# Kernel tuning notes

Measured on AMD Instinct MI355X. Metric: run time of the kernel, lower is better.

## Reference

```python
import jax, jax.numpy as jnp
import numpy as np

B, N = 2048, 4095  # batch, number of spherical points (cumsum length = N+1)


def setup_inputs() -> dict:
    key = jax.random.key(0)
    k1, k2, k3, k4, k5 = jax.random.split(key, 5)
    return {
        "origin_3D": jax.random.uniform(k1, (B, 3, 1), dtype=jnp.float32),
        "spherical_3D": jax.random.uniform(k2, (B, 3, N), dtype=jnp.float32),
        "origin_2D": jax.random.uniform(k3, (B, 3, 1), dtype=jnp.float32),
        "spherical_2D": jax.random.uniform(k4, (B, 3, N), dtype=jnp.float32),
        "deformation_field": jax.random.uniform(k5, (B, 2, N), dtype=jnp.float32),
    }


def _cart(origin, spherical):
    # spherical: [B, 3, N] with rows (r, theta, phi)
    r, theta, phi = spherical[:, 0, :], spherical[:, 1, :], spherical[:, 2, :]
    st = jnp.sin(theta)
    x = r * st * jnp.cos(phi)
    y = r * st * jnp.sin(phi)
    z = r * jnp.cos(theta)
    shape = jnp.stack((x, y, z), axis=1)            # [B, 3, N]
    full = jnp.concatenate((origin, shape), axis=2)  # [B, 3, N+1]
    # torch.matmul(full, triu(ones)) == prefix sum along the last axis
    return jnp.cumsum(full, axis=2)


def reference(origin_3D, spherical_3D, origin_2D, spherical_2D, deformation_field):
    spherical_3D_deformed = spherical_3D.at[:, 1:, :].add(deformation_field)
    original_cart = _cart(origin_2D, spherical_2D)            # [B, 3, N+1]
    deformed_cart = _cart(origin_3D, spherical_3D_deformed)   # [B, 3, N+1]
    per_pt = jnp.sum(jnp.abs(deformed_cart - original_cart), axis=1)  # [B, N+1]
    return jnp.sum(jnp.mean(per_pt, axis=1))  # scalar
```

## Files before the change

kernel.cpp:

```cpp
#include <hip/hip_runtime.h>


#define BATCH 2048
#define NPTS  4095
#define POS   4096
#define T     256
#define CHUNK 16
#define PAD   17

__global__ void zero_out_kernel(float* out) { out[0] = 0.0f; }

__launch_bounds__(T)
__global__ void mpd_loss_kernel(const float* __restrict__ origin3,
                                const float* __restrict__ sph3,
                                const float* __restrict__ origin2,
                                const float* __restrict__ sph2,
                                const float* __restrict__ def,
                                float* __restrict__ out) {
    __shared__ float dX[T * PAD];
    __shared__ float dY[T * PAD];
    __shared__ float dZ[T * PAD];
    __shared__ float totX[T], totY[T], totZ[T];
    __shared__ float wsum[T / 64];

    const int b = blockIdx.x;
    const int t = threadIdx.x;

    const float* r3  = sph3 + (size_t)b * 3 * NPTS;
    const float* th3 = r3 + NPTS;
    const float* ph3 = th3 + NPTS;
    const float* r2  = sph2 + (size_t)b * 3 * NPTS;
    const float* th2 = r2 + NPTS;
    const float* ph2 = th2 + NPTS;
    const float* d0  = def + (size_t)b * 2 * NPTS;
    const float* d1  = d0 + NPTS;

    #pragma unroll 4
    for (int m = 0; m < CHUNK; ++m) {
        const int j = m * T + t;
        float dx, dy, dz;
        if (j == 0) {
            const float* o3 = origin3 + (size_t)b * 3;
            const float* o2 = origin2 + (size_t)b * 3;
            dx = o3[0] - o2[0];
            dy = o3[1] - o2[1];
            dz = o3[2] - o2[2];
        } else {
            const int n = j - 1;
            const float R3  = r3[n];
            const float Th3 = th3[n] + d0[n];
            const float Ph3 = ph3[n] + d1[n];
            const float R2  = r2[n];
            const float Th2 = th2[n];
            const float Ph2 = ph2[n];
            float s3, c3, sp3, cp3, s2, c2, sp2, cp2;
            __sincosf(Th3, &s3, &c3);
            __sincosf(Ph3, &sp3, &cp3);
            __sincosf(Th2, &s2, &c2);
            __sincosf(Ph2, &sp2, &cp2);
            const float rs3 = R3 * s3;
            const float rs2 = R2 * s2;
            dx = rs3 * cp3 - rs2 * cp2;
            dy = rs3 * sp3 - rs2 * sp2;
            dz = R3 * c3 - R2 * c2;
        }
        const int addr = (j >> 4) * PAD + (j & 15);
        dX[addr] = dx;
        dY[addr] = dy;
        dZ[addr] = dz;
    }
    __syncthreads();

    const int base = t * PAD;
    float sx = 0.f, sy = 0.f, sz = 0.f;
    #pragma unroll
    for (int k = 0; k < CHUNK; ++k) {
        sx += dX[base + k];
        sy += dY[base + k];
        sz += dZ[base + k];
    }
    totX[t] = sx; totY[t] = sy; totZ[t] = sz;
    __syncthreads();

    for (int off = 1; off < T; off <<= 1) {
        float vx = 0.f, vy = 0.f, vz = 0.f;
        if (t >= off) { vx = totX[t - off]; vy = totY[t - off]; vz = totZ[t - off]; }
        __syncthreads();
        totX[t] += vx; totY[t] += vy; totZ[t] += vz;
        __syncthreads();
    }
    const float ox = totX[t] - sx;
    const float oy = totY[t] - sy;
    const float oz = totZ[t] - sz;

    float acc = 0.f;
    float px = ox, py = oy, pz = oz;
    #pragma unroll
    for (int k = 0; k < CHUNK; ++k) {
        px += dX[base + k];
        py += dY[base + k];
        pz += dZ[base + k];
        acc += fabsf(px) + fabsf(py) + fabsf(pz);
    }

    #pragma unroll
    for (int off = 32; off > 0; off >>= 1) acc += __shfl_down(acc, off, 64);
    if ((t & 63) == 0) wsum[t >> 6] = acc;
    __syncthreads();
    if (t == 0) {
        const float s = wsum[0] + wsum[1] + wsum[2] + wsum[3];
        atomicAdd(out, s * (1.0f / POS));
    }
}

extern "C" void kernel_launch(void* const* d_in, const int* in_sizes, int n_in,
                              void* d_out, int out_size, void* d_ws, size_t ws_size,
                              hipStream_t stream) {
    const float* origin3 = (const float*)d_in[0];
    const float* sph3    = (const float*)d_in[1];
    const float* origin2 = (const float*)d_in[2];
    const float* sph2    = (const float*)d_in[3];
    const float* def     = (const float*)d_in[4];
    float* out = (float*)d_out;

    zero_out_kernel<<<1, 1, 0, stream>>>(out);
    mpd_loss_kernel<<<BATCH, T, 0, stream>>>(origin3, sph3, origin2, sph2, def, out);
}
```

Measured before the change: 271.5 us.

## Replace LDS-staged block scan with register-held wavefront shuffle scans

The prefix sum no longer stages all 4096 per-point deltas in padded shared memory and runs a multi-barrier Hillis-Steele scan. Each thread keeps its 16 deltas in registers, each wavefront scans them with shuffle-up steps, and only the per-wave totals go through a small LDS table. That table is combined into block offsets after a single barrier. This removes most LDS traffic and barriers, but adds many shuffle instructions and raises register pressure, and the launch bound now requests 4 blocks per multiprocessor.

New measurement: 281.3 us. 1.04x slower.

```diff
diff --git a/kernel.cpp b/kernel.cpp
--- a/kernel.cpp
+++ b/kernel.cpp
@@ -5,26 +5,25 @@
 #define NPTS  4095
 #define POS   4096
 #define T     256
-#define CHUNK 16
-#define PAD   17
+#define NW    4
+#define M     16
 
 __global__ void zero_out_kernel(float* out) { out[0] = 0.0f; }
 
-__launch_bounds__(T)
+__launch_bounds__(T, 4)
 __global__ void mpd_loss_kernel(const float* __restrict__ origin3,
                                 const float* __restrict__ sph3,
                                 const float* __restrict__ origin2,
                                 const float* __restrict__ sph2,
                                 const float* __restrict__ def,
                                 float* __restrict__ out) {
-    __shared__ float dX[T * PAD];
-    __shared__ float dY[T * PAD];
-    __shared__ float dZ[T * PAD];
-    __shared__ float totX[T], totY[T], totZ[T];
-    __shared__ float wsum[T / 64];
+    __shared__ float ldsT[3][M][NW];
+    __shared__ float wsum[NW];
 
-    const int b = blockIdx.x;
-    const int t = threadIdx.x;
+    const int b    = blockIdx.x;
+    const int t    = threadIdx.x;
+    const int lane = t & 63;
+    const int w    = t >> 6;
 
     const float* r3  = sph3 + (size_t)b * 3 * NPTS;
     const float* th3 = r3 + NPTS;
@@ -35,8 +34,10 @@
     const float* d0  = def + (size_t)b * 2 * NPTS;
     const float* d1  = d0 + NPTS;
 
-    #pragma unroll 4
-    for (int m = 0; m < CHUNK; ++m) {
+    float vx[M], vy[M], vz[M];
+
+    #pragma unroll
+    for (int m = 0; m < M; ++m) {
         const int j = m * T + t;
         float dx, dy, dz;
         if (j == 0) {
@@ -64,52 +65,52 @@
             dy = rs3 * sp3 - rs2 * sp2;
             dz = R3 * c3 - R2 * c2;
         }
-        const int addr = (j >> 4) * PAD + (j & 15);
-        dX[addr] = dx;
-        dY[addr] = dy;
-        dZ[addr] = dz;
+        vx[m] = dx; vy[m] = dy; vz[m] = dz;
+    }
+
+    #pragma unroll
+    for (int m = 0; m < M; ++m) {
+        float x = vx[m], y = vy[m], z = vz[m];
+        #pragma unroll
+        for (int off = 1; off < 64; off <<= 1) {
+            const float ux = __shfl_up(x, off, 64);
+            const float uy = __shfl_up(y, off, 64);
+            const float uz = __shfl_up(z, off, 64);
+            if (lane >= off) { x += ux; y += uy; z += uz; }
+        }
+        vx[m] = x; vy[m] = y; vz[m] = z;
+        if (lane == 63) {
+            ldsT[0][m][w] = x;
+            ldsT[1][m][w] = y;
+            ldsT[2][m][w] = z;
+        }
     }
     __syncthreads();
 
-    const int base = t * PAD;
-    float sx = 0.f, sy = 0.f, sz = 0.f;
+    float acc = 0.f;
+    float rbx = 0.f, rby = 0.f, rbz = 0.f;
     #pragma unroll
-    for (int k = 0; k < CHUNK; ++k) {
-        sx += dX[base + k];
-        sy += dY[base + k];
-        sz += dZ[base + k];
-    }
-    totX[t] = sx; totY[t] = sy; totZ[t] = sz;
-    __syncthreads();
-
-    for (int off = 1; off < T; off <<= 1) {
-        float vx = 0.f, vy = 0.f, vz = 0.f;
-        if (t >= off) { vx = totX[t - off]; vy = totY[t - off]; vz = totZ[t - off]; }
-        __syncthreads();
-        totX[t] += vx; totY[t] += vy; totZ[t] += vz;
-        __syncthreads();
-    }
-    const float ox = totX[t] - sx;
-    const float oy = totY[t] - sy;
-    const float oz = totZ[t] - sz;
-
-    float acc = 0.f;
-    float px = ox, py = oy, pz = oz;
-    #pragma unroll
-    for (int k = 0; k < CHUNK; ++k) {
-        px += dX[base + k];
-        py += dY[base + k];
-        pz += dZ[base + k];
-        acc += fabsf(px) + fabsf(py) + fabsf(pz);
+    for (int m = 0; m < M; ++m) {
+        float wx = 0.f, wy = 0.f, wz = 0.f;
+        float tx = 0.f, ty = 0.f, tz = 0.f;
+        #pragma unroll
+        for (int ww = 0; ww < NW; ++ww) {
+            const float a = ldsT[0][m][ww];
+            const float c = ldsT[1][m][ww];
+            const float e = ldsT[2][m][ww];
+            if (ww < w) { wx += a; wy += c; wz += e; }
+            tx += a; ty += c; tz += e;
+        }
+        acc += fabsf(rbx + wx + vx[m]) + fabsf(rby + wy + vy[m]) + fabsf(rbz + wz + vz[m]);
+        rbx += tx; rby += ty; rbz += tz;
     }
 
     #pragma unroll
     for (int off = 32; off > 0; off >>= 1) acc += __shfl_down(acc, off, 64);
-    if ((t & 63) == 0) wsum[t >> 6] = acc;
+    if (lane == 0) wsum[w] = acc;
     __syncthreads();
     if (t == 0) {
-        const float s = wsum[0] + wsum[1] + wsum[2] + wsum[3];
-        atomicAdd(out, s * (1.0f / POS));
+        atomicAdd(out, (wsum[0] + wsum[1] + wsum[2] + wsum[3]) * (1.0f / POS));
     }
 }
 
```
